# Optimization experiments

Measured on AMD Instinct MI355X. Metric: run time of the kernel, lower is better.

Reference implementation:

```python
import jax, jax.numpy as jnp
import numpy as np

# Cell hyperparameters (from model.cell / Eprop_fit.__init__)
THRESHOLD = 0.6
DAMPENING = 0.3
N_REF = 5
DECAY = 0.8          # membrane decay used for pre-synaptic trace filters
ELIG_DECAY = 0.8     # default decay in exp_convolve for eligibility filtering
REG = 300.0


def exp_convolve(t, decay):
    """Causal exponential filter along time axis 1: a_t = decay*a_{t-1} + x_t."""
    xt = jnp.moveaxis(t, 1, 0)  # time-major [T, B, ...]

    def step(acc, cur):
        acc = acc * decay + cur
        return acc, acc

    _, y = jax.lax.scan(step, jnp.zeros_like(xt[0]), xt)
    return jnp.moveaxis(y, 0, 1)


def refractory_count(z, n_ref):
    """ref_count[t] depends on z[:t]; starts at 0."""
    zt = jnp.moveaxis(jax.lax.stop_gradient(z), 1, 0)  # [T, B, N]
    init = jnp.zeros(zt.shape[1:], jnp.int32)

    def step(c, zc):
        c = jnp.where(zc > 0, jnp.int32(n_ref - 1), jnp.maximum(0, c - 1))
        return c, c

    _, counts = jax.lax.scan(step, init, zt[:-1])
    counts = jnp.concatenate([init[None], counts], axis=0)
    return jnp.moveaxis(counts, 0, 1)  # [B, T, N]


def setup_inputs() -> dict:
    key = jax.random.key(0)
    k1, k2, k3, k4, k5, k6 = jax.random.split(key, 6)
    B, T, N, NIN, K = 4, 300, 200, 100, 10
    v = jax.random.normal(k1, (B, T, N), jnp.float32) * 0.5 + 0.3
    z = (jax.random.uniform(k2, (B, T, N)) < 0.05).astype(jnp.float32)  # spikes
    x = (jax.random.uniform(k3, (B, T, NIN)) < 0.1).astype(jnp.float32)
    error1 = jax.random.normal(k4, (B, T, K), jnp.float32) * 0.1   # output error
    error2 = jax.random.normal(k5, (N,), jnp.float32) * 0.01       # firing-rate error
    w_out = jax.random.normal(k6, (N, K), jnp.float32) / np.sqrt(N)
    return {"v": v, "z": z, "x": x, "error1": error1, "error2": error2, "w_out": w_out}


def reference(v, z, x, error1, error2, w_out):
    B, T, N = v.shape

    v_scaled = (v - THRESHOLD) / THRESHOLD
    psi_no_ref = DAMPENING * jnp.maximum(1.0 - jnp.abs(v_scaled), 0.0) / THRESHOLD

    ref = refractory_count(z, N_REF)
    post_term = jnp.where(ref > 0, 0.0, psi_no_ref)  # [B, T, N]

    # shift z by one time step (z_{t-1}, zero-initialized)
    z_prev = jnp.concatenate([jnp.zeros_like(z[:, :1]), z[:, :-1]], axis=1)

    pre_w_in = exp_convolve(x, DECAY)        # x_bar  [B, T, n_in]
    pre_w_rec = exp_convolve(z_prev, DECAY)  # z_bar  [B, T, N]
    pre_w_out = exp_convolve(z, DECAY)       # [B, T, N]

    # eligibility traces: [B, T, pre, post]
    et_in = post_term[:, :, None, :] * pre_w_in[:, :, :, None]
    et_rec = post_term[:, :, None, :] * pre_w_rec[:, :, :, None]

    fet_in = exp_convolve(et_in, ELIG_DECAY)
    fet_rec = exp_convolve(et_rec, ELIG_DECAY)

    avg_in = jnp.mean(et_in, axis=(0, 1))    # [n_in, N]
    avg_rec = jnp.mean(et_rec, axis=(0, 1))  # [N, N]

    # learning signals (symmetric e-prop): L = error @ w_out^T
    learning_signals = jnp.einsum('btk,jk->btj', error1, w_out)  # [B, T, N]

    dloss_dw_out = jnp.einsum('btk,btj->jk', error1, pre_w_out)          # [N, K]
    dloss_dw_in = jnp.einsum('btj,btij->ij', learning_signals, fet_in)   # [n_in, N]
    dloss_dw_rec = jnp.einsum('btj,btij->ij', learning_signals, fet_rec) # [N, N]

    dloss_dw_in = dloss_dw_in + REG * (error2 * avg_in)
    dloss_dw_rec = dloss_dw_rec + REG * (error2 * avg_rec)

    # mask autapses (diagonal of recurrent weight gradient)
    eye = jnp.eye(N, dtype=bool)
    dloss_dw_rec = jnp.where(eye, 0.0, dloss_dw_rec)

    return dloss_dw_in, dloss_dw_rec, dloss_dw_out
```

## Files before the change

kernel.cpp:

```cpp
#include <hip/hip_runtime.h>

#define BB    4
#define TT    300
#define NN    200
#define NINN  100
#define KK    10
#define DECAY 0.8f
#define THR   0.6f
#define DAMP  0.3f

#define LCH   20
#define NCHK  (TT / LCH)
#define WARM  48

#define XBAR_OFF  0
#define ZFILT_OFF (BB*TT*NINN)
#define ZBAR_OFF  (ZFILT_OFF + BB*TT*NN)
#define CBUF_OFF  (ZBAR_OFF  + BB*TT*NN)

#define NB_A 24
#define NB_B 47
#define NB_C 240
#define CB_BASE  (NB_A + NB_B)
#define ZB_BASE  (CB_BASE + NB_C)
#define NB_TOTAL (ZB_BASE + 2)

__global__ void fused_kernel(const float* __restrict__ v,
                             const float* __restrict__ z,
                             const float* __restrict__ x,
                             const float* __restrict__ error1,
                             const float* __restrict__ error2,
                             const float* __restrict__ w_out,
                             float* __restrict__ ws,
                             float* __restrict__ out) {
    int bid = blockIdx.x;
    int tid = threadIdx.x;
    float* xbar  = ws + XBAR_OFF;
    float* zfilt = ws + ZFILT_OFF;
    float* zbar  = ws + ZBAR_OFF;
    float* cbuf  = ws + CBUF_OFF;

    if (bid < NB_A) {
        int u = bid * 256 + tid;
        if (u < BB * NCHK * NINN) {
            int i = u % NINN, r = u / NINN;
            int chunk = r % NCHK, b = r / NCHK;
            int t0 = chunk * LCH;
            const float* src = x + (size_t)b * TT * NINN + i;
            float acc = 0.f;
            #pragma unroll
            for (int d = WARM; d >= 1; --d) {
                int t = t0 - d;
                int tc = t < 0 ? 0 : t;
                float val = src[tc * NINN];
                acc = DECAY * acc + (t < 0 ? 0.f : val);
            }
            float vals[LCH];
            #pragma unroll
            for (int tt = 0; tt < LCH; ++tt) vals[tt] = src[(t0 + tt) * NINN];
            #pragma unroll
            for (int tt = 0; tt < LCH; ++tt) { acc = DECAY * acc + vals[tt]; vals[tt] = acc; }
            float* dst = xbar + (size_t)b * TT * NINN + i;
            #pragma unroll
            for (int tt = 0; tt < LCH; ++tt) dst[(t0 + tt) * NINN] = vals[tt];
        }
    } else if (bid < CB_BASE) {
        int u = (bid - NB_A) * 256 + tid;
        if (u < BB * NCHK * NN) {
            int j = u % NN, r = u / NN;
            int chunk = r % NCHK, b = r / NCHK;
            int t0 = chunk * LCH;
            const float* src = z + (size_t)b * TT * NN + j;
            float acc = 0.f;
            #pragma unroll
            for (int d = WARM; d >= 1; --d) {
                int t = t0 - d;
                int tc = t < 0 ? 0 : t;
                float val = src[tc * NN];
                acc = DECAY * acc + (t < 0 ? 0.f : val);
            }
            float zv[LCH], pre[LCH];
            #pragma unroll
            for (int tt = 0; tt < LCH; ++tt) zv[tt] = src[(t0 + tt) * NN];
            #pragma unroll
            for (int tt = 0; tt < LCH; ++tt) {
                pre[tt] = acc;
                acc = DECAY * acc + zv[tt];
                zv[tt] = acc;
            }
            float* dzb = zbar  + (size_t)b * TT * NN + j;
            float* dzf = zfilt + (size_t)b * TT * NN + j;
            #pragma unroll
            for (int tt = 0; tt < LCH; ++tt) dzb[(t0 + tt) * NN] = pre[tt];
            #pragma unroll
            for (int tt = 0; tt < LCH; ++tt) dzf[(t0 + tt) * NN] = zv[tt];
        }
    } else if (bid < ZB_BASE) {
        __shared__ float gl[5][KK];
        int cb = bid - CB_BASE;
        int bt0 = cb * 5;
        int b = bt0 / TT;
        int t0 = bt0 - b * TT;
        if (tid < 5 * KK) {
            int btl = tid / KK, k = tid - btl * KK;
            int t = t0 + btl;
            const float* src = error1 + (size_t)b * TT * KK + k;
            float G = 0.f;
            #pragma unroll
            for (int d = WARM - 1; d >= 0; --d) {
                int s = t + d;
                int sc = s > TT - 1 ? TT - 1 : s;
                float val = src[sc * KK];
                G = DECAY * G + (s > TT - 1 ? 0.f : val);
            }
            gl[btl][k] = G;
        }
        __syncthreads();
        if (tid < 250) {
            int jq = tid % 50, btl = tid / 50;
            int t = t0 + btl;
            int bt = bt0 + btl;
            int j0 = jq * 4;

            float g[KK];
            #pragma unroll
            for (int k = 0; k < KK; ++k) g[k] = gl[btl][k];

            float Ld[4];
            #pragma unroll
            for (int a = 0; a < 4; ++a) {
                const float* wr = w_out + (j0 + a) * KK;
                float acc = 0.f;
                #pragma unroll
                for (int k = 0; k < KK; ++k) acc += g[k] * wr[k];
                Ld[a] = acc;
            }

            float4 e2v = *(const float4*)(error2 + j0);
            float co[4] = {0.25f * e2v.x, 0.25f * e2v.y, 0.25f * e2v.z, 0.25f * e2v.w};

            bool refr[4] = {false, false, false, false};
            #pragma unroll
            for (int d = 1; d <= 4; ++d) {
                int s = t - d;
                int sc = s < 0 ? 0 : s;
                float4 zv = *(const float4*)(z + ((size_t)b * TT + sc) * NN + j0);
                if (s >= 0) {
                    if (zv.x > 0.f) refr[0] = true;
                    if (zv.y > 0.f) refr[1] = true;
                    if (zv.z > 0.f) refr[2] = true;
                    if (zv.w > 0.f) refr[3] = true;
                }
            }

            float4 vv = *(const float4*)(v + (size_t)bt * NN + j0);
            float vm[4] = {vv.x, vv.y, vv.z, vv.w};
            float cm[4];
            #pragma unroll
            for (int a = 0; a < 4; ++a) {
                float vs = (vm[a] - THR) / THR;
                float psi = (DAMP / THR) * fmaxf(1.f - fabsf(vs), 0.f);
                cm[a] = (refr[a] ? 0.f : psi) * (Ld[a] + co[a]);
            }
            *(float4*)(cbuf + (size_t)bt * NN + j0) = make_float4(cm[0], cm[1], cm[2], cm[3]);
        }
    } else {
        int u = (bid - ZB_BASE) * 256 + tid;
        if (u < 500)
            ((float4*)(out + NINN * NN + NN * NN))[u] = make_float4(0.f, 0.f, 0.f, 0.f);
    }
}

#define SKB 16
#define KC3 (BB * TT / SKB)
#define PT  4
#define JT  64

__global__ void out_kernel(const float* __restrict__ error1,
                           const float* __restrict__ ws,
                           float* __restrict__ out) {
    __shared__ float red[SKB * PT * JT];
    int bid = blockIdx.x;
    int tid = threadIdx.x;
    const float* xbar  = ws + XBAR_OFF;
    const float* zfilt = ws + ZFILT_OFF;
    const float* zbar  = ws + ZBAR_OFF;
    const float* cbuf  = ws + CBUF_OFF;

    if (bid < 300) {
        int pt = bid >> 2;
        int jt = bid & 3;
        int p0 = pt * PT;
        int j0 = jt * JT;
        int W = NN - j0; if (W > JT) W = JT;
        int jq = tid & 15;
        int s  = tid >> 4;

        if (jq * 4 < W) {
            bool isrec = (p0 >= NINN);
            const float* A = isrec ? (zbar + (p0 - NINN)) : (xbar + p0);
            int lda = isrec ? NN : NINN;
            const float* C = cbuf + j0 + jq * 4;
            int bt0 = s * KC3;
            float acc[4][4];
            #pragma unroll
            for (int a = 0; a < 4; ++a)
                #pragma unroll
                for (int c = 0; c < 4; ++c) acc[a][c] = 0.f;
            #pragma unroll 5
            for (int rr = 0; rr < KC3; ++rr) {
                int bt = bt0 + rr;
                float4 av = *(const float4*)(A + (size_t)bt * lda);
                float4 cv = *(const float4*)(C + (size_t)bt * NN);
                float am[4] = {av.x, av.y, av.z, av.w};
                float cm[4] = {cv.x, cv.y, cv.z, cv.w};
                #pragma unroll
                for (int a = 0; a < 4; ++a)
                    #pragma unroll
                    for (int c = 0; c < 4; ++c) acc[a][c] += am[a] * cm[c];
            }
            float* dst = red + s * (PT * JT) + jq * 4;
            #pragma unroll
            for (int a = 0; a < 4; ++a)
                *(float4*)(dst + a * JT) =
                    make_float4(acc[a][0], acc[a][1], acc[a][2], acc[a][3]);
        }
        __syncthreads();

        int o = tid;
        int pl = o >> 6, jl = o & 63;
        if (jl < W) {
            float sum = 0.f;
            #pragma unroll
            for (int s2 = 0; s2 < SKB; ++s2) sum += red[s2 * (PT * JT) + o];
            int row = p0 + pl;
            int j = j0 + jl;
            if (row < NINN) {
                out[row * NN + j] = sum;
            } else {
                int i = row - NINN;
                out[NINN * NN + i * NN + j] = (i == j) ? 0.f : sum;
            }
        }
    } else {
        int u = (bid - 300) * 256 + tid;
        if (u < 6 * NN * KK) {
            int jk = u % (NN * KK);
            int s = u / (NN * KK);
            int j = jk % NN;
            int k = jk / NN;
            int bt0 = s * 200;
            float acc = 0.f;
            #pragma unroll 8
            for (int rr = 0; rr < 200; ++rr) {
                int bt = bt0 + rr;
                acc += zfilt[bt * NN + j] * error1[bt * KK + k];
            }
            atomicAdd(out + NINN * NN + NN * NN + j * KK + k, acc);
        }
    }
}

extern "C" void kernel_launch(void* const* d_in, const int* in_sizes, int n_in,
                              void* d_out, int out_size, void* d_ws, size_t ws_size,
                              hipStream_t stream) {
    const float* v  = (const float*)d_in[0];
    const float* z  = (const float*)d_in[1];
    const float* x  = (const float*)d_in[2];
    const float* e1 = (const float*)d_in[3];
    const float* e2 = (const float*)d_in[4];
    const float* wo = (const float*)d_in[5];
    float* out = (float*)d_out;
    float* ws  = (float*)d_ws;

    fused_kernel<<<NB_TOTAL, 256, 0, stream>>>(v, z, x, e1, e2, wo, ws, out);

    out_kernel<<<347, 256, 0, stream>>>(e1, ws, out);
}
```

Measured before the change: 85.56 us.

## Merge two kernels into one cooperative kernel with grid sync

Combines the producer and consumer kernels into a single cooperative launch separated by a grid-wide barrier, which removes one kernel launch and its gap. It also changes the output-weight gradient: it now uses a reverse-time filtered error against raw spikes, written to per-block partials and reduced without atomics. That removes the zfilt buffer and the zeroing pass. The cost is grid-sync overhead, cooperative launch limits on the number of co-resident blocks (323 blocks of 256 threads), and a larger static shared-memory footprint for every block.

```diff
diff --git a/kernel.cpp b/kernel.cpp
--- a/kernel.cpp
+++ b/kernel.cpp
@@ -1,4 +1,7 @@
 #include <hip/hip_runtime.h>
+#include <hip/hip_cooperative_groups.h>
+
+namespace cg = cooperative_groups;
 
 #define BB    4
 #define TT    300
@@ -17,28 +20,37 @@
 #define ZFILT_OFF (BB*TT*NINN)
 #define ZBAR_OFF  (ZFILT_OFF + BB*TT*NN)
 #define CBUF_OFF  (ZBAR_OFF  + BB*TT*NN)
+#define PART_OFF  (CBUF_OFF  + BB*TT*NN)
 
 #define NB_A 24
 #define NB_B 47
 #define NB_C 240
 #define CB_BASE  (NB_A + NB_B)
-#define ZB_BASE  (CB_BASE + NB_C)
-#define NB_TOTAL (ZB_BASE + 2)
-
-__global__ void fused_kernel(const float* __restrict__ v,
-                             const float* __restrict__ z,
-                             const float* __restrict__ x,
-                             const float* __restrict__ error1,
-                             const float* __restrict__ error2,
-                             const float* __restrict__ w_out,
-                             float* __restrict__ ws,
-                             float* __restrict__ out) {
+#define DB_BASE  (CB_BASE + NB_C)
+#define NB_D 12
+#define NBLK (DB_BASE + NB_D)
+
+
+#define SKB 16
+#define KC3 (BB * TT / SKB)
+#define PT  4
+#define JT  64
+
+__global__ void coop_kernel(const float* __restrict__ v,
+                            const float* __restrict__ z,
+                            const float* __restrict__ x,
+                            const float* __restrict__ error1,
+                            const float* __restrict__ error2,
+                            const float* __restrict__ w_out,
+                            float* __restrict__ ws,
+                            float* __restrict__ out) {
+    __shared__ float smem[SKB * PT * JT];
     int bid = blockIdx.x;
     int tid = threadIdx.x;
-    float* xbar  = ws + XBAR_OFF;
-    float* zfilt = ws + ZFILT_OFF;
-    float* zbar  = ws + ZBAR_OFF;
-    float* cbuf  = ws + CBUF_OFF;
+    float* xbar = ws + XBAR_OFF;
+    float* zbar = ws + ZBAR_OFF;
+    float* cbuf = ws + CBUF_OFF;
+    float* part = ws + PART_OFF;
 
     if (bid < NB_A) {
         int u = bid * 256 + tid;
@@ -86,17 +98,12 @@
             for (int tt = 0; tt < LCH; ++tt) {
                 pre[tt] = acc;
                 acc = DECAY * acc + zv[tt];
-                zv[tt] = acc;
-            }
-            float* dzb = zbar  + (size_t)b * TT * NN + j;
-            float* dzf = zfilt + (size_t)b * TT * NN + j;
+            }
+            float* dzb = zbar + (size_t)b * TT * NN + j;
             #pragma unroll
             for (int tt = 0; tt < LCH; ++tt) dzb[(t0 + tt) * NN] = pre[tt];
-            #pragma unroll
-            for (int tt = 0; tt < LCH; ++tt) dzf[(t0 + tt) * NN] = zv[tt];
-        }
-    } else if (bid < ZB_BASE) {
-        __shared__ float gl[5][KK];
+        }
+    } else if (bid < DB_BASE) {
         int cb = bid - CB_BASE;
         int bt0 = cb * 5;
         int b = bt0 / TT;
@@ -113,7 +120,7 @@
                 float val = src[sc * KK];
                 G = DECAY * G + (s > TT - 1 ? 0.f : val);
             }
-            gl[btl][k] = G;
+            smem[btl * KK + k] = G;
         }
         __syncthreads();
         if (tid < 250) {
@@ -124,7 +131,7 @@
 
             float g[KK];
             #pragma unroll
-            for (int k = 0; k < KK; ++k) g[k] = gl[btl][k];
+            for (int k = 0; k < KK; ++k) g[k] = smem[btl * KK + k];
 
             float Ld[4];
             #pragma unroll
@@ -165,27 +172,45 @@
             *(float4*)(cbuf + (size_t)bt * NN + j0) = make_float4(cm[0], cm[1], cm[2], cm[3]);
         }
     } else {
-        int u = (bid - ZB_BASE) * 256 + tid;
-        if (u < 500)
-            ((float4*)(out + NINN * NN + NN * NN))[u] = make_float4(0.f, 0.f, 0.f, 0.f);
+        int s = bid - DB_BASE;
+        int b = s / 3;
+        int t0 = (s % 3) * 100;
+        if (tid < KK) {
+            const float* src = error1 + (size_t)b * TT * KK + tid;
+            float G = 0.f;
+            #pragma unroll
+            for (int d = WARM; d >= 1; --d) {
+                int t = t0 + 99 + d;
+                int tc = t > TT - 1 ? TT - 1 : t;
+                float val = src[tc * KK];
+                G = DECAY * G + (t > TT - 1 ? 0.f : val);
+            }
+            #pragma unroll 4
+            for (int tt = 99; tt >= 0; --tt) {
+                G = DECAY * G + src[(t0 + tt) * KK];
+                smem[tt * KK + tid] = G;
+            }
+        }
+        __syncthreads();
+        if (tid < NN) {
+            const float* zp = z + ((size_t)b * TT + t0) * NN + tid;
+            float acc[KK];
+            #pragma unroll
+            for (int k = 0; k < KK; ++k) acc[k] = 0.f;
+            #pragma unroll 4
+            for (int tt = 0; tt < 100; ++tt) {
+                float zv = zp[tt * NN];
+                #pragma unroll
+                for (int k = 0; k < KK; ++k) acc[k] += zv * smem[tt * KK + k];
+            }
+            float* pd = part + s * (NN * KK) + tid * KK;
+            #pragma unroll
+            for (int k = 0; k < KK; ++k) pd[k] = acc[k];
+        }
     }
-}
-
-#define SKB 16
-#define KC3 (BB * TT / SKB)
-#define PT  4
-#define JT  64
-
-__global__ void out_kernel(const float* __restrict__ error1,
-                           const float* __restrict__ ws,
-                           float* __restrict__ out) {
-    __shared__ float red[SKB * PT * JT];
-    int bid = blockIdx.x;
-    int tid = threadIdx.x;
-    const float* xbar  = ws + XBAR_OFF;
-    const float* zfilt = ws + ZFILT_OFF;
-    const float* zbar  = ws + ZBAR_OFF;
-    const float* cbuf  = ws + CBUF_OFF;
+
+    __threadfence();
+    cg::this_grid().sync();
 
     if (bid < 300) {
         int pt = bid >> 2;
@@ -194,14 +219,15 @@
         int j0 = jt * JT;
         int W = NN - j0; if (W > JT) W = JT;
         int jq = tid & 15;
-        int s  = tid >> 4;
-
+        int sg = tid >> 4;
+
+        __syncthreads();
         if (jq * 4 < W) {
             bool isrec = (p0 >= NINN);
             const float* A = isrec ? (zbar + (p0 - NINN)) : (xbar + p0);
             int lda = isrec ? NN : NINN;
             const float* C = cbuf + j0 + jq * 4;
-            int bt0 = s * KC3;
+            int bt0 = sg * KC3;
             float acc[4][4];
             #pragma unroll
             for (int a = 0; a < 4; ++a)
@@ -219,7 +245,7 @@
                     #pragma unroll
                     for (int c = 0; c < 4; ++c) acc[a][c] += am[a] * cm[c];
             }
-            float* dst = red + s * (PT * JT) + jq * 4;
+            float* dst = smem + sg * (PT * JT) + jq * 4;
             #pragma unroll
             for (int a = 0; a < 4; ++a)
                 *(float4*)(dst + a * JT) =
@@ -232,7 +258,7 @@
         if (jl < W) {
             float sum = 0.f;
             #pragma unroll
-            for (int s2 = 0; s2 < SKB; ++s2) sum += red[s2 * (PT * JT) + o];
+            for (int s2 = 0; s2 < SKB; ++s2) sum += smem[s2 * (PT * JT) + o];
             int row = p0 + pl;
             int j = j0 + jl;
             if (row < NINN) {
@@ -242,21 +268,13 @@
                 out[NINN * NN + i * NN + j] = (i == j) ? 0.f : sum;
             }
         }
-    } else {
+    } else if (bid < 308) {
         int u = (bid - 300) * 256 + tid;
-        if (u < 6 * NN * KK) {
-            int jk = u % (NN * KK);
-            int s = u / (NN * KK);
-            int j = jk % NN;
-            int k = jk / NN;
-            int bt0 = s * 200;
-            float acc = 0.f;
-            #pragma unroll 8
-            for (int rr = 0; rr < 200; ++rr) {
-                int bt = bt0 + rr;
-                acc += zfilt[bt * NN + j] * error1[bt * KK + k];
-            }
-            atomicAdd(out + NINN * NN + NN * NN + j * KK + k, acc);
+        if (u < NN * KK) {
+            float sum = 0.f;
+            #pragma unroll
+            for (int p = 0; p < NB_D; ++p) sum += part[p * (NN * KK) + u];
+            out[NINN * NN + NN * NN + u] = sum;
         }
     }
 }
@@ -273,7 +291,8 @@
     float* out = (float*)d_out;
     float* ws  = (float*)d_ws;
 
-    fused_kernel<<<NB_TOTAL, 256, 0, stream>>>(v, z, x, e1, e2, wo, ws, out);
-
-    out_kernel<<<347, 256, 0, stream>>>(e1, ws, out);
+    void* args[] = {(void*)&v, (void*)&z, (void*)&x, (void*)&e1,
+                    (void*)&e2, (void*)&wo, (void*)&ws, (void*)&out};
+    hipLaunchCooperativeKernel((const void*)coop_kernel, dim3(NBLK), dim3(256),
+                               args, 0, stream);
 }
```

Result: slower. 188.0 us (+119.7%).
